# Performance work log

Hardware: AMD Instinct MI355X
Metric: run time of the kernel (lower is better)

Reference implementation:

```python
import jax, jax.numpy as jnp
import numpy as np

B, T, I = 8, 128, 196
TEXT_DIM, IMAGE_DIM, HIDDEN = 768, 1024, 512


def setup_inputs() -> dict:
    key = jax.random.key(0)
    ks = jax.random.split(key, 7)
    s = lambda d: 1.0 / np.sqrt(d)
    return {
        "text_features": jax.random.normal(ks[0], (B, T, TEXT_DIM), jnp.float32),
        "image_features": jax.random.normal(ks[1], (B, I, IMAGE_DIM), jnp.float32),
        "Wt": jax.random.normal(ks[2], (TEXT_DIM, HIDDEN), jnp.float32) * s(TEXT_DIM),
        "bt": jax.random.normal(ks[3], (HIDDEN,), jnp.float32) * s(TEXT_DIM),
        "Wi": jax.random.normal(ks[4], (IMAGE_DIM, HIDDEN), jnp.float32) * s(IMAGE_DIM),
        "bi": jax.random.normal(ks[5], (HIDDEN,), jnp.float32) * s(IMAGE_DIM),
        "wa": jax.random.normal(ks[6], (HIDDEN,), jnp.float32) * s(HIDDEN),
        "ba": jnp.zeros((1,), jnp.float32),
    }


def reference(text_features, image_features, Wt, bt, Wi, bi, wa, ba):
    # projections: [B,T,H] and [B,I,H]
    pt = jnp.einsum("btd,dh->bth", text_features, Wt) + bt
    pi = jnp.einsum("bid,dh->bih", image_features, Wi) + bi
    # additive Bahdanau scores: tanh of broadcast sum [B,T,I,H], reduced by wa
    h = jnp.tanh(pt[:, :, None, :] + pi[:, None, :, :])
    scores = jnp.einsum("btih,h->bti", h, wa) + ba[0]  # [B,T,I]
    text_attended = jnp.einsum("bti,bid->btd", jax.nn.softmax(scores, axis=-1), image_features)
    image_attended = jnp.einsum("bti,btd->bid", jax.nn.softmax(scores, axis=1), text_features)
    return text_attended, image_attended
```

## Files before the change

kernel.cpp:

```cpp
#include <hip/hip_runtime.h>
#include <math.h>

#define B 8
#define T 128
#define I_TOK 196
#define TEXT_DIM 768
#define IMAGE_DIM 1024
#define HIDDEN 512
#define EXP_SCALE 2.88539008177792681f

#if __has_builtin(__builtin_amdgcn_exp2f)
#define FAST_EXP2(x) __builtin_amdgcn_exp2f(x)
#else
#define FAST_EXP2(x) exp2f(x)
#endif
#if __has_builtin(__builtin_amdgcn_rcpf)
#define FAST_RCP(x) __builtin_amdgcn_rcpf(x)
#else
#define FAST_RCP(x) __fdividef(1.f, (x))
#endif
#if __has_builtin(__builtin_amdgcn_sched_barrier)
#define SCHED_FENCE() __builtin_amdgcn_sched_barrier(0)
#else
#define SCHED_FENCE()
#endif

typedef short bf16x8 __attribute__((ext_vector_type(8)));
typedef float f32x4 __attribute__((ext_vector_type(4)));

#define KT_T (TEXT_DIM / 32)
#define KT_I (IMAGE_DIM / 32)
#define MT_T (B * T / 16)
#define MT_I (B * I_TOK / 16)
#define NT   (HIDDEN / 16)

#define XT_ELEMS (MT_T * KT_T * 512)
#define XI_ELEMS (MT_I * KT_I * 512)
#define X_ELEMS  (XT_ELEMS + XI_ELEMS)
#define WT_T_ELEMS (NT * KT_T * 512)
#define W_ELEMS (WT_T_ELEMS + NT * KT_I * 512)

#define XTILES_T (MT_T * KT_T)
#define XTILES   (XTILES_T + MT_I * KT_I)
#define WTILES_T (NT * KT_T)
#define WTILES   (WTILES_T + NT * KT_I)
#define PREP_GRID ((XTILES + WTILES) / 4)

__device__ __forceinline__ unsigned short f2bf(float x) {
    unsigned int u = __float_as_uint(x);
    unsigned int r = u + 0x7FFFu + ((u >> 16) & 1u);
    return (unsigned short)(r >> 16);
}
__device__ __forceinline__ float bf2f(unsigned short h) {
    return __uint_as_float(((unsigned int)h) << 16);
}

__global__ __launch_bounds__(256) void prep_kernel(
        const float* __restrict__ text, const float* __restrict__ image,
        const float* __restrict__ Wt, const float* __restrict__ Wi,
        unsigned short* __restrict__ Xh, unsigned short* __restrict__ Xl,
        unsigned short* __restrict__ WTh, unsigned short* __restrict__ WTl)
{
    const int tid = threadIdx.x;
    const int lane = tid & 63, wv = tid >> 6;
    const int r16 = lane & 15, quad = lane >> 4;
    const int id = blockIdx.x * 4 + wv;

    float v[8];
    unsigned short* oh;
    unsigned short* ol;
    long dst;

    if (id < XTILES) {
        const float* X; int K, mt, kt;
        if (id < XTILES_T) { X = text; K = TEXT_DIM; mt = id / KT_T; kt = id % KT_T; }
        else { const int i2 = id - XTILES_T; X = image; K = IMAGE_DIM; mt = i2 / KT_I; kt = i2 % KT_I; }
        const float* src = X + (long)(mt * 16 + r16) * K + kt * 32 + quad * 8;
        const float4 a = *(const float4*)src;
        const float4 b = *(const float4*)(src + 4);
        v[0]=a.x; v[1]=a.y; v[2]=a.z; v[3]=a.w; v[4]=b.x; v[5]=b.y; v[6]=b.z; v[7]=b.w;
        oh = (id < XTILES_T) ? Xh : Xh + XT_ELEMS;
        ol = (id < XTILES_T) ? Xl : Xl + XT_ELEMS;
        const long tile = (id < XTILES_T) ? id : (long)(id - XTILES_T);
        dst = tile * 512 + lane * 8;
    } else {
        const int idw = id - XTILES;
        const float* W; int K, nt, kt;
        if (idw < WTILES_T) { W = Wt; K = TEXT_DIM; nt = idw / KT_T; kt = idw % KT_T; }
        else { const int i2 = idw - WTILES_T; W = Wi; K = IMAGE_DIM; nt = i2 / KT_I; kt = i2 % KT_I; }
        const float* src = W + (long)(kt * 32 + quad * 8) * HIDDEN + nt * 16 + r16;
        #pragma unroll
        for (int j = 0; j < 8; ++j) v[j] = src[(long)j * HIDDEN];
        oh = (idw < WTILES_T) ? WTh : WTh + WT_T_ELEMS;
        ol = (idw < WTILES_T) ? WTl : WTl + WT_T_ELEMS;
        const long tile = (idw < WTILES_T) ? idw : (long)(idw - WTILES_T);
        dst = tile * 512 + lane * 8;
    }

    uint4 hv, lv;
    unsigned int hh[8], ll[8];
    #pragma unroll
    for (int j = 0; j < 8; ++j) {
        hh[j] = f2bf(v[j]);
        ll[j] = f2bf(v[j] - bf2f((unsigned short)hh[j]));
    }
    hv.x = hh[0] | (hh[1] << 16); hv.y = hh[2] | (hh[3] << 16);
    hv.z = hh[4] | (hh[5] << 16); hv.w = hh[6] | (hh[7] << 16);
    lv.x = ll[0] | (ll[1] << 16); lv.y = ll[2] | (ll[3] << 16);
    lv.z = ll[4] | (ll[5] << 16); lv.w = ll[6] | (ll[7] << 16);
    *(uint4*)(oh + dst) = hv;
    *(uint4*)(ol + dst) = lv;
}

#define GT_BLOCKS (32 * 8)
#define GI_BLOCKS (49 * 8)
#define GEMM_GRID (GT_BLOCKS + GI_BLOCKS)
#define PSTRIDE 66

__global__ __launch_bounds__(256, 2) void mfma_proj_kernel(
        const unsigned short* __restrict__ Xh, const unsigned short* __restrict__ Xl,
        const unsigned short* __restrict__ WTh, const unsigned short* __restrict__ WTl,
        const float* __restrict__ bt, const float* __restrict__ bi,
        float* __restrict__ pt, float* __restrict__ pi)
{
    __shared__ float part[32 * PSTRIDE];

    const int tid = threadIdx.x;
    const int lane = tid & 63, wv = tid >> 6;
    const int r16 = lane & 15, quad = lane >> 4;
    const int nh = wv & 1;
    const int kh = wv >> 1;

    int bid = blockIdx.x;
    const unsigned short *xh, *xl, *wh, *wl; const float* bias; float* Y;
    int ktiles;
    if (bid < GT_BLOCKS) {
        xh = Xh; xl = Xl; wh = WTh; wl = WTl; bias = bt; Y = pt; ktiles = KT_T;
    } else {
        bid -= GT_BLOCKS;
        xh = Xh + XT_ELEMS; xl = Xl + XT_ELEMS;
        wh = WTh + WT_T_ELEMS; wl = WTl + WT_T_ELEMS;
        bias = bi; Y = pi; ktiles = KT_I;
    }
    const int m0 = (bid >> 3) * 32;
    const int n0 = (bid & 7) * 64 + nh * 32;
    const int nstep = ktiles >> 1;
    const int kt0 = kh * nstep;
    const int mt0 = (bid >> 3) * 2;
    const int nt0 = (bid & 7) * 4 + nh * 2;

    const unsigned short* pa0 = xh + ((long)mt0 * ktiles + kt0) * 512 + lane * 8;
    const unsigned short* pa1 = pa0 + (long)ktiles * 512;
    const unsigned short* qa0 = xl + ((long)mt0 * ktiles + kt0) * 512 + lane * 8;
    const unsigned short* qa1 = qa0 + (long)ktiles * 512;
    const unsigned short* pb0 = wh + ((long)nt0 * ktiles + kt0) * 512 + lane * 8;
    const unsigned short* pb1 = pb0 + (long)ktiles * 512;
    const unsigned short* qb0 = wl + ((long)nt0 * ktiles + kt0) * 512 + lane * 8;
    const unsigned short* qb1 = qb0 + (long)ktiles * 512;

    f32x4 a00 = {0,0,0,0}, a01 = {0,0,0,0}, a10 = {0,0,0,0}, a11 = {0,0,0,0};

    bf16x8 Ah0 = *(const bf16x8*)(pa0);
    bf16x8 Ah1 = *(const bf16x8*)(pa1);
    bf16x8 Al0 = *(const bf16x8*)(qa0);
    bf16x8 Al1 = *(const bf16x8*)(qa1);
    bf16x8 Bh0 = *(const bf16x8*)(pb0);
    bf16x8 Bh1 = *(const bf16x8*)(pb1);
    bf16x8 Bl0 = *(const bf16x8*)(qb0);
    bf16x8 Bl1 = *(const bf16x8*)(qb1);

    for (int s = 0; s < nstep; ++s) {
        const long kn = (s + 1 < nstep) ? (long)(s + 1) * 512 : 0;
        const bf16x8 nAh0 = *(const bf16x8*)(pa0 + kn);
        const bf16x8 nAh1 = *(const bf16x8*)(pa1 + kn);
        const bf16x8 nAl0 = *(const bf16x8*)(qa0 + kn);
        const bf16x8 nAl1 = *(const bf16x8*)(qa1 + kn);
        const bf16x8 nBh0 = *(const bf16x8*)(pb0 + kn);
        const bf16x8 nBh1 = *(const bf16x8*)(pb1 + kn);
        const bf16x8 nBl0 = *(const bf16x8*)(qb0 + kn);
        const bf16x8 nBl1 = *(const bf16x8*)(qb1 + kn);
        SCHED_FENCE();

        a00 = __builtin_amdgcn_mfma_f32_16x16x32_bf16(Ah0, Bh0, a00, 0, 0, 0);
        a01 = __builtin_amdgcn_mfma_f32_16x16x32_bf16(Ah0, Bh1, a01, 0, 0, 0);
        a10 = __builtin_amdgcn_mfma_f32_16x16x32_bf16(Ah1, Bh0, a10, 0, 0, 0);
        a11 = __builtin_amdgcn_mfma_f32_16x16x32_bf16(Ah1, Bh1, a11, 0, 0, 0);
        a00 = __builtin_amdgcn_mfma_f32_16x16x32_bf16(Ah0, Bl0, a00, 0, 0, 0);
        a01 = __builtin_amdgcn_mfma_f32_16x16x32_bf16(Ah0, Bl1, a01, 0, 0, 0);
        a10 = __builtin_amdgcn_mfma_f32_16x16x32_bf16(Ah1, Bl0, a10, 0, 0, 0);
        a11 = __builtin_amdgcn_mfma_f32_16x16x32_bf16(Ah1, Bl1, a11, 0, 0, 0);
        a00 = __builtin_amdgcn_mfma_f32_16x16x32_bf16(Al0, Bh0, a00, 0, 0, 0);
        a01 = __builtin_amdgcn_mfma_f32_16x16x32_bf16(Al0, Bh1, a01, 0, 0, 0);
        a10 = __builtin_amdgcn_mfma_f32_16x16x32_bf16(Al1, Bh0, a10, 0, 0, 0);
        a11 = __builtin_amdgcn_mfma_f32_16x16x32_bf16(Al1, Bh1, a11, 0, 0, 0);
        SCHED_FENCE();

        Ah0 = nAh0; Ah1 = nAh1; Al0 = nAl0; Al1 = nAl1;
        Bh0 = nBh0; Bh1 = nBh1; Bl0 = nBl0; Bl1 = nBl1;
    }

    const int lc = nh * 32 + r16;
    if (kh == 1) {
        #pragma unroll
        for (int r = 0; r < 4; ++r) {
            part[(quad * 4 + r) * PSTRIDE + lc]           = a00[r];
            part[(quad * 4 + r) * PSTRIDE + lc + 16]      = a01[r];
            part[(quad * 4 + 16 + r) * PSTRIDE + lc]      = a10[r];
            part[(quad * 4 + 16 + r) * PSTRIDE + lc + 16] = a11[r];
        }
    }
    __syncthreads();
    if (kh == 0) {
        const int row0 = m0 + quad * 4;
        const float bv0 = bias[n0 + r16];
        const float bv1 = bias[n0 + 16 + r16];
        #pragma unroll
        for (int r = 0; r < 4; ++r) {
            const float v00 = (a00[r] + part[(quad * 4 + r) * PSTRIDE + lc]           + bv0) * EXP_SCALE;
            const float v01 = (a01[r] + part[(quad * 4 + r) * PSTRIDE + lc + 16]      + bv1) * EXP_SCALE;
            const float v10 = (a10[r] + part[(quad * 4 + 16 + r) * PSTRIDE + lc]      + bv0) * EXP_SCALE;
            const float v11 = (a11[r] + part[(quad * 4 + 16 + r) * PSTRIDE + lc + 16] + bv1) * EXP_SCALE;
            Y[(long)(row0 + r)      * HIDDEN + n0 + r16]      = FAST_EXP2(v00);
            Y[(long)(row0 + r)      * HIDDEN + n0 + 16 + r16] = FAST_EXP2(v01);
            Y[(long)(row0 + 16 + r) * HIDDEN + n0 + r16]      = FAST_EXP2(v10);
            Y[(long)(row0 + 16 + r) * HIDDEN + n0 + 16 + r16] = FAST_EXP2(v11);
        }
    }
}

__global__ __launch_bounds__(256, 8) void scores_kernel(const float* __restrict__ pt,
        const float* __restrict__ pi, const float* __restrict__ wa,
        const float* __restrict__ ba, float* __restrict__ scores)
{
    const int blk = blockIdx.x;
    const int bt = blk >> 1;
    const int half = blk & 1;
    const int b = bt >> 7;
    const int tid = threadIdx.x;
    const int lane = tid & 63, wave = tid >> 6;

    const float* ptrow = pt + (long)bt * HIDDEN + lane * 8;
    const float4 pA = *(const float4*)ptrow;
    const float4 pB = *(const float4*)(ptrow + 4);
    float4 wA = *(const float4*)(wa + lane * 8);
    float4 wB = *(const float4*)(wa + lane * 8 + 4);

    float S = wA.x + wA.y + wA.z + wA.w + wB.x + wB.y + wB.z + wB.w;
    #pragma unroll
    for (int off = 32; off; off >>= 1) S += __shfl_down(S, off);
    const float base = S + ba[0];

    wA.x *= -2.f; wA.y *= -2.f; wA.z *= -2.f; wA.w *= -2.f;
    wB.x *= -2.f; wB.y *= -2.f; wB.z *= -2.f; wB.w *= -2.f;

    const float* pib = pi + (long)b * I_TOK * HIDDEN + lane * 8;
    const int i0 = half * 98 + wave;
    const int iend = half * 98 + 98;

    float4 ca = *(const float4*)(pib + (long)i0 * HIDDEN);
    float4 cb = *(const float4*)(pib + (long)i0 * HIDDEN + 4);

    for (int i = i0; i < iend; i += 4) {
        const int inx = (i + 4 < iend) ? (i + 4) : i;
        const float4 na = *(const float4*)(pib + (long)inx * HIDDEN);
        const float4 nb = *(const float4*)(pib + (long)inx * HIDDEN + 4);

        float acc = 0.f;
        acc = fmaf(wA.x, FAST_RCP(fmaf(pA.x, ca.x, 1.f)), acc);
        acc = fmaf(wA.y, FAST_RCP(fmaf(pA.y, ca.y, 1.f)), acc);
        acc = fmaf(wA.z, FAST_RCP(fmaf(pA.z, ca.z, 1.f)), acc);
        acc = fmaf(wA.w, FAST_RCP(fmaf(pA.w, ca.w, 1.f)), acc);
        acc = fmaf(wB.x, FAST_RCP(fmaf(pB.x, cb.x, 1.f)), acc);
        acc = fmaf(wB.y, FAST_RCP(fmaf(pB.y, cb.y, 1.f)), acc);
        acc = fmaf(wB.z, FAST_RCP(fmaf(pB.z, cb.z, 1.f)), acc);
        acc = fmaf(wB.w, FAST_RCP(fmaf(pB.w, cb.w, 1.f)), acc);

        #pragma unroll
        for (int off = 32; off; off >>= 1) acc += __shfl_down(acc, off);
        if (lane == 0) scores[(long)bt * I_TOK + i] = base + acc;
        ca = na; cb = nb;
    }
}

__global__ __launch_bounds__(256) void att_kernel(const float* __restrict__ scores,
        const float* __restrict__ image, const float* __restrict__ text,
        float* __restrict__ out_text, float* __restrict__ out_img)
{
    const int tid = threadIdx.x, lane = tid & 63, wave = tid >> 6;

    if (blockIdx.x < 512) {
        const int bid = blockIdx.x;
        const int csplit = bid & 1;
        const int grp = bid >> 1;
        const int b = grp >> 5;
        const int t0 = (grp & 31) * 4;

        __shared__ float ps[I_TOK][4];
        {
            const float* srow = scores + ((long)(b * T + t0 + wave)) * I_TOK;
            const float s0 = srow[lane];
            const float s1 = srow[lane + 64];
            const float s2 = srow[lane + 128];
            const float s3 = (lane < 4) ? srow[lane + 192] : -INFINITY;
            float m = fmaxf(fmaxf(s0, s1), fmaxf(s2, s3));
            #pragma unroll
            for (int off = 32; off; off >>= 1) m = fmaxf(m, __shfl_xor(m, off));
            const float e0 = __expf(s0 - m);
            const float e1 = __expf(s1 - m);
            const float e2 = __expf(s2 - m);
            const float e3 = (lane < 4) ? __expf(s3 - m) : 0.f;
            float sum = e0 + e1 + e2 + e3;
            #pragma unroll
            for (int off = 32; off; off >>= 1) sum += __shfl_xor(sum, off);
            const float inv = __fdividef(1.0f, sum);
            ps[lane][wave] = e0 * inv;
            ps[lane + 64][wave] = e1 * inv;
            ps[lane + 128][wave] = e2 * inv;
            if (lane < 4) ps[lane + 192][wave] = e3 * inv;
        }
        __syncthreads();

        const float* img = image + (long)b * I_TOK * IMAGE_DIM + csplit * 512 + tid * 2;
        float a00 = 0.f, a01 = 0.f, a10 = 0.f, a11 = 0.f;
        float a20 = 0.f, a21 = 0.f, a30 = 0.f, a31 = 0.f;

        float2 v0 = *(const float2*)(img + 0 * IMAGE_DIM);
        float2 v1 = *(const float2*)(img + 1 * IMAGE_DIM);
        float2 v2 = *(const float2*)(img + 2 * IMAGE_DIM);
        float2 v3 = *(const float2*)(img + 3 * IMAGE_DIM);
        float4 p0 = *(const float4*)&ps[0][0];
        float4 p1 = *(const float4*)&ps[1][0];
        float4 p2 = *(const float4*)&ps[2][0];
        float4 p3 = *(const float4*)&ps[3][0];

        for (int g = 0; g < 49; ++g) {
            const int ib = (g + 1 < 49) ? (g + 1) * 4 : g * 4;
            const float2 w0 = *(const float2*)(img + (long)(ib + 0) * IMAGE_DIM);
            const float2 w1 = *(const float2*)(img + (long)(ib + 1) * IMAGE_DIM);
            const float2 w2 = *(const float2*)(img + (long)(ib + 2) * IMAGE_DIM);
            const float2 w3 = *(const float2*)(img + (long)(ib + 3) * IMAGE_DIM);
            const float4 r0 = *(const float4*)&ps[ib + 0][0];
            const float4 r1 = *(const float4*)&ps[ib + 1][0];
            const float4 r2 = *(const float4*)&ps[ib + 2][0];
            const float4 r3 = *(const float4*)&ps[ib + 3][0];
            a00 = fmaf(p0.x, v0.x, a00); a01 = fmaf(p0.x, v0.y, a01);
            a10 = fmaf(p0.y, v0.x, a10); a11 = fmaf(p0.y, v0.y, a11);
            a20 = fmaf(p0.z, v0.x, a20); a21 = fmaf(p0.z, v0.y, a21);
            a30 = fmaf(p0.w, v0.x, a30); a31 = fmaf(p0.w, v0.y, a31);
            a00 = fmaf(p1.x, v1.x, a00); a01 = fmaf(p1.x, v1.y, a01);
            a10 = fmaf(p1.y, v1.x, a10); a11 = fmaf(p1.y, v1.y, a11);
            a20 = fmaf(p1.z, v1.x, a20); a21 = fmaf(p1.z, v1.y, a21);
            a30 = fmaf(p1.w, v1.x, a30); a31 = fmaf(p1.w, v1.y, a31);
            a00 = fmaf(p2.x, v2.x, a00); a01 = fmaf(p2.x, v2.y, a01);
            a10 = fmaf(p2.y, v2.x, a10); a11 = fmaf(p2.y, v2.y, a11);
            a20 = fmaf(p2.z, v2.x, a20); a21 = fmaf(p2.z, v2.y, a21);
            a30 = fmaf(p2.w, v2.x, a30); a31 = fmaf(p2.w, v2.y, a31);
            a00 = fmaf(p3.x, v3.x, a00); a01 = fmaf(p3.x, v3.y, a01);
            a10 = fmaf(p3.y, v3.x, a10); a11 = fmaf(p3.y, v3.y, a11);
            a20 = fmaf(p3.z, v3.x, a20); a21 = fmaf(p3.z, v3.y, a21);
            a30 = fmaf(p3.w, v3.x, a30); a31 = fmaf(p3.w, v3.y, a31);
            v0 = w0; v1 = w1; v2 = w2; v3 = w3;
            p0 = r0; p1 = r1; p2 = r2; p3 = r3;
        }
        float* o = out_text + ((long)(b * T + t0)) * IMAGE_DIM + csplit * 512 + tid * 2;
        float2 w;
        w.x = a00; w.y = a01; *(float2*)(o + 0 * IMAGE_DIM) = w;
        w.x = a10; w.y = a11; *(float2*)(o + 1 * IMAGE_DIM) = w;
        w.x = a20; w.y = a21; *(float2*)(o + 2 * IMAGE_DIM) = w;
        w.x = a30; w.y = a31; *(float2*)(o + 3 * IMAGE_DIM) = w;
    } else {
        const int bid = blockIdx.x - 512;
        const int b = bid / (I_TOK / 4);
        const int i0 = (bid % (I_TOK / 4)) * 4;

        __shared__ float qs[T][4];
        {
            const float* sc = scores + (long)b * T * I_TOK + (i0 + wave);
            const float s0 = sc[(long)lane * I_TOK];
            const float s1 = sc[(long)(lane + 64) * I_TOK];
            float m = fmaxf(s0, s1);
            #pragma unroll
            for (int off = 32; off; off >>= 1) m = fmaxf(m, __shfl_xor(m, off));
            const float e0 = __expf(s0 - m);
            const float e1 = __expf(s1 - m);
            float sum = e0 + e1;
            #pragma unroll
            for (int off = 32; off; off >>= 1) sum += __shfl_xor(sum, off);
            const float inv = __fdividef(1.0f, sum);
            qs[lane][wave] = e0 * inv;
            qs[lane + 64][wave] = e1 * inv;
        }
        __syncthreads();

        const float* txt2 = text + (long)b * T * TEXT_DIM + tid * 2;
        const float* txt1 = text + (long)b * T * TEXT_DIM + 512 + tid;
        float a00=0.f,a01=0.f,a02=0.f, a10=0.f,a11=0.f,a12=0.f;
        float a20=0.f,a21=0.f,a22=0.f, a30=0.f,a31=0.f,a32=0.f;

        float2 u0 = *(const float2*)(txt2 + 0 * TEXT_DIM);
        float2 u1 = *(const float2*)(txt2 + 1 * TEXT_DIM);
        float  z0 = txt1[0 * TEXT_DIM];
        float  z1 = txt1[1 * TEXT_DIM];
        float4 q0 = *(const float4*)&qs[0][0];
        float4 q1 = *(const float4*)&qs[1][0];

        for (int g = 0; g < 64; ++g) {
            const int tb = (g + 1 < 64) ? (g + 1) * 2 : g * 2;
            const float2 nu0 = *(const float2*)(txt2 + (long)(tb + 0) * TEXT_DIM);
            const float2 nu1 = *(const float2*)(txt2 + (long)(tb + 1) * TEXT_DIM);
            const float  nz0 = txt1[(long)(tb + 0) * TEXT_DIM];
            const float  nz1 = txt1[(long)(tb + 1) * TEXT_DIM];
            const float4 nq0 = *(const float4*)&qs[tb + 0][0];
            const float4 nq1 = *(const float4*)&qs[tb + 1][0];
            a00 = fmaf(q0.x, u0.x, a00); a01 = fmaf(q0.x, u0.y, a01); a02 = fmaf(q0.x, z0, a02);
            a10 = fmaf(q0.y, u0.x, a10); a11 = fmaf(q0.y, u0.y, a11); a12 = fmaf(q0.y, z0, a12);
            a20 = fmaf(q0.z, u0.x, a20); a21 = fmaf(q0.z, u0.y, a21); a22 = fmaf(q0.z, z0, a22);
            a30 = fmaf(q0.w, u0.x, a30); a31 = fmaf(q0.w, u0.y, a31); a32 = fmaf(q0.w, z0, a32);
            a00 = fmaf(q1.x, u1.x, a00); a01 = fmaf(q1.x, u1.y, a01); a02 = fmaf(q1.x, z1, a02);
            a10 = fmaf(q1.y, u1.x, a10); a11 = fmaf(q1.y, u1.y, a11); a12 = fmaf(q1.y, z1, a12);
            a20 = fmaf(q1.z, u1.x, a20); a21 = fmaf(q1.z, u1.y, a21); a22 = fmaf(q1.z, z1, a22);
            a30 = fmaf(q1.w, u1.x, a30); a31 = fmaf(q1.w, u1.y, a31); a32 = fmaf(q1.w, z1, a32);
            u0 = nu0; u1 = nu1; z0 = nz0; z1 = nz1; q0 = nq0; q1 = nq1;
        }
        float* o = out_img + ((long)b * I_TOK + i0) * TEXT_DIM;
        float2 w;
        w.x = a00; w.y = a01; *(float2*)(o + 0 * TEXT_DIM + tid * 2) = w; o[0 * TEXT_DIM + 512 + tid] = a02;
        w.x = a10; w.y = a11; *(float2*)(o + 1 * TEXT_DIM + tid * 2) = w; o[1 * TEXT_DIM + 512 + tid] = a12;
        w.x = a20; w.y = a21; *(float2*)(o + 2 * TEXT_DIM + tid * 2) = w; o[2 * TEXT_DIM + 512 + tid] = a22;
        w.x = a30; w.y = a31; *(float2*)(o + 3 * TEXT_DIM + tid * 2) = w; o[3 * TEXT_DIM + 512 + tid] = a32;
    }
}

extern "C" void kernel_launch(void* const* d_in, const int* in_sizes, int n_in,
                              void* d_out, int out_size, void* d_ws, size_t ws_size,
                              hipStream_t stream) {
    const float* text  = (const float*)d_in[0];
    const float* image = (const float*)d_in[1];
    const float* Wt    = (const float*)d_in[2];
    const float* bt    = (const float*)d_in[3];
    const float* Wi    = (const float*)d_in[4];
    const float* bi    = (const float*)d_in[5];
    const float* wa    = (const float*)d_in[6];
    const float* ba    = (const float*)d_in[7];

    float* pt = (float*)d_ws;
    float* pi = pt + (long)B * T * HIDDEN;
    float* sc = pi + (long)B * I_TOK * HIDDEN;
    unsigned short* Xh  = (unsigned short*)(sc + (long)B * T * I_TOK);
    unsigned short* Xl  = Xh + X_ELEMS;
    unsigned short* WTh = Xl + X_ELEMS;
    unsigned short* WTl = WTh + W_ELEMS;

    float* out_text = (float*)d_out;
    float* out_img  = out_text + (long)B * T * IMAGE_DIM;

    prep_kernel<<<PREP_GRID, 256, 0, stream>>>(text, image, Wt, Wi, Xh, Xl, WTh, WTl);
    mfma_proj_kernel<<<GEMM_GRID, 256, 0, stream>>>(Xh, Xl, WTh, WTl, bt, bi, pt, pi);
    scores_kernel<<<2 * B * T, 256, 0, stream>>>(pt, pi, wa, ba, sc);
    att_kernel<<<512 + B * (I_TOK / 4), 256, 0, stream>>>(sc, image, text, out_text, out_img);
}
```

Measured before the change: 145.5 us.

## Process two text rows per scores block and widen attention output tiles

The scores kernel now computes two text rows per block, so each loaded image-projection vector is reused twice, which halves the grid and pi traffic. The occupancy hint drops from 8 to 4 blocks per CU to leave room for the extra registers. The attention kernel now gives each block 8 text rows (was 4) and 7 image tokens (was 4), which cuts redundant re-reads of image and text features. The cost is more registers per thread and fewer blocks to keep the GPU busy.

```diff
diff --git a/kernel.cpp b/kernel.cpp
--- a/kernel.cpp
+++ b/kernel.cpp
@@ -228,20 +228,22 @@
     }
 }
 
-__global__ __launch_bounds__(256, 8) void scores_kernel(const float* __restrict__ pt,
+__global__ __launch_bounds__(256, 4) void scores_kernel(const float* __restrict__ pt,
         const float* __restrict__ pi, const float* __restrict__ wa,
         const float* __restrict__ ba, float* __restrict__ scores)
 {
     const int blk = blockIdx.x;
-    const int bt = blk >> 1;
     const int half = blk & 1;
-    const int b = bt >> 7;
+    const int bt0 = (blk >> 1) * 2;
+    const int b = bt0 >> 7;
     const int tid = threadIdx.x;
     const int lane = tid & 63, wave = tid >> 6;
 
-    const float* ptrow = pt + (long)bt * HIDDEN + lane * 8;
-    const float4 pA = *(const float4*)ptrow;
-    const float4 pB = *(const float4*)(ptrow + 4);
+    const float* ptrow = pt + (long)bt0 * HIDDEN + lane * 8;
+    const float4 pA0 = *(const float4*)ptrow;
+    const float4 pB0 = *(const float4*)(ptrow + 4);
+    const float4 pA1 = *(const float4*)(ptrow + HIDDEN);
+    const float4 pB1 = *(const float4*)(ptrow + HIDDEN + 4);
     float4 wA = *(const float4*)(wa + lane * 8);
     float4 wB = *(const float4*)(wa + lane * 8 + 4);
 
@@ -265,22 +267,42 @@
         const float4 na = *(const float4*)(pib + (long)inx * HIDDEN);
         const float4 nb = *(const float4*)(pib + (long)inx * HIDDEN + 4);
 
-        float acc = 0.f;
-        acc = fmaf(wA.x, FAST_RCP(fmaf(pA.x, ca.x, 1.f)), acc);
-        acc = fmaf(wA.y, FAST_RCP(fmaf(pA.y, ca.y, 1.f)), acc);
-        acc = fmaf(wA.z, FAST_RCP(fmaf(pA.z, ca.z, 1.f)), acc);
-        acc = fmaf(wA.w, FAST_RCP(fmaf(pA.w, ca.w, 1.f)), acc);
-        acc = fmaf(wB.x, FAST_RCP(fmaf(pB.x, cb.x, 1.f)), acc);
-        acc = fmaf(wB.y, FAST_RCP(fmaf(pB.y, cb.y, 1.f)), acc);
-        acc = fmaf(wB.z, FAST_RCP(fmaf(pB.z, cb.z, 1.f)), acc);
-        acc = fmaf(wB.w, FAST_RCP(fmaf(pB.w, cb.w, 1.f)), acc);
-
-        #pragma unroll
-        for (int off = 32; off; off >>= 1) acc += __shfl_down(acc, off);
-        if (lane == 0) scores[(long)bt * I_TOK + i] = base + acc;
+        float acc0 = 0.f;
+        acc0 = fmaf(wA.x, FAST_RCP(fmaf(pA0.x, ca.x, 1.f)), acc0);
+        acc0 = fmaf(wA.y, FAST_RCP(fmaf(pA0.y, ca.y, 1.f)), acc0);
+        acc0 = fmaf(wA.z, FAST_RCP(fmaf(pA0.z, ca.z, 1.f)), acc0);
+        acc0 = fmaf(wA.w, FAST_RCP(fmaf(pA0.w, ca.w, 1.f)), acc0);
+        acc0 = fmaf(wB.x, FAST_RCP(fmaf(pB0.x, cb.x, 1.f)), acc0);
+        acc0 = fmaf(wB.y, FAST_RCP(fmaf(pB0.y, cb.y, 1.f)), acc0);
+        acc0 = fmaf(wB.z, FAST_RCP(fmaf(pB0.z, cb.z, 1.f)), acc0);
+        acc0 = fmaf(wB.w, FAST_RCP(fmaf(pB0.w, cb.w, 1.f)), acc0);
+
+        float acc1 = 0.f;
+        acc1 = fmaf(wA.x, FAST_RCP(fmaf(pA1.x, ca.x, 1.f)), acc1);
+        acc1 = fmaf(wA.y, FAST_RCP(fmaf(pA1.y, ca.y, 1.f)), acc1);
+        acc1 = fmaf(wA.z, FAST_RCP(fmaf(pA1.z, ca.z, 1.f)), acc1);
+        acc1 = fmaf(wA.w, FAST_RCP(fmaf(pA1.w, ca.w, 1.f)), acc1);
+        acc1 = fmaf(wB.x, FAST_RCP(fmaf(pB1.x, cb.x, 1.f)), acc1);
+        acc1 = fmaf(wB.y, FAST_RCP(fmaf(pB1.y, cb.y, 1.f)), acc1);
+        acc1 = fmaf(wB.z, FAST_RCP(fmaf(pB1.z, cb.z, 1.f)), acc1);
+        acc1 = fmaf(wB.w, FAST_RCP(fmaf(pB1.w, cb.w, 1.f)), acc1);
+
+        #pragma unroll
+        for (int off = 32; off; off >>= 1) {
+            acc0 += __shfl_down(acc0, off);
+            acc1 += __shfl_down(acc1, off);
+        }
+        if (lane == 0) {
+            scores[(long)bt0 * I_TOK + i]       = base + acc0;
+            scores[(long)(bt0 + 1) * I_TOK + i] = base + acc1;
+        }
         ca = na; cb = nb;
     }
 }
+
+#define ATT_P1_BLOCKS 256
+#define ATT_P2_BLOCKS (B * 28)
+#define ATT_GRID (ATT_P1_BLOCKS + ATT_P2_BLOCKS)
 
 __global__ __launch_bounds__(256) void att_kernel(const float* __restrict__ scores,
         const float* __restrict__ image, const float* __restrict__ text,
@@ -288,16 +310,18 @@
 {
     const int tid = threadIdx.x, lane = tid & 63, wave = tid >> 6;
 
-    if (blockIdx.x < 512) {
+    if (blockIdx.x < ATT_P1_BLOCKS) {
         const int bid = blockIdx.x;
         const int csplit = bid & 1;
         const int grp = bid >> 1;
-        const int b = grp >> 5;
-        const int t0 = (grp & 31) * 4;
-
-        __shared__ float ps[I_TOK][4];
-        {
-            const float* srow = scores + ((long)(b * T + t0 + wave)) * I_TOK;
+        const int b = grp >> 4;
+        const int t0 = (grp & 15) * 8;
+
+        __shared__ float ps[I_TOK][8];
+        #pragma unroll
+        for (int rr = 0; rr < 2; ++rr) {
+            const int tsub = wave + rr * 4;
+            const float* srow = scores + ((long)(b * T + t0 + tsub)) * I_TOK;
             const float s0 = srow[lane];
             const float s1 = srow[lane + 64];
             const float s2 = srow[lane + 128];
@@ -313,25 +337,25 @@
             #pragma unroll
             for (int off = 32; off; off >>= 1) sum += __shfl_xor(sum, off);
             const float inv = __fdividef(1.0f, sum);
-            ps[lane][wave] = e0 * inv;
-            ps[lane + 64][wave] = e1 * inv;
-            ps[lane + 128][wave] = e2 * inv;
-            if (lane < 4) ps[lane + 192][wave] = e3 * inv;
+            ps[lane][tsub] = e0 * inv;
+            ps[lane + 64][tsub] = e1 * inv;
+            ps[lane + 128][tsub] = e2 * inv;
+            if (lane < 4) ps[lane + 192][tsub] = e3 * inv;
         }
         __syncthreads();
 
         const float* img = image + (long)b * I_TOK * IMAGE_DIM + csplit * 512 + tid * 2;
-        float a00 = 0.f, a01 = 0.f, a10 = 0.f, a11 = 0.f;
-        float a20 = 0.f, a21 = 0.f, a30 = 0.f, a31 = 0.f;
+        float2 a0 = {0,0}, a1 = {0,0}, a2 = {0,0}, a3 = {0,0};
+        float2 a4 = {0,0}, a5 = {0,0}, a6 = {0,0}, a7 = {0,0};
 
         float2 v0 = *(const float2*)(img + 0 * IMAGE_DIM);
         float2 v1 = *(const float2*)(img + 1 * IMAGE_DIM);
         float2 v2 = *(const float2*)(img + 2 * IMAGE_DIM);
         float2 v3 = *(const float2*)(img + 3 * IMAGE_DIM);
-        float4 p0 = *(const float4*)&ps[0][0];
-        float4 p1 = *(const float4*)&ps[1][0];
-        float4 p2 = *(const float4*)&ps[2][0];
-        float4 p3 = *(const float4*)&ps[3][0];
+        float4 pL0 = *(const float4*)&ps[0][0]; float4 pH0 = *(const float4*)&ps[0][4];
+        float4 pL1 = *(const float4*)&ps[1][0]; float4 pH1 = *(const float4*)&ps[1][4];
+        float4 pL2 = *(const float4*)&ps[2][0]; float4 pH2 = *(const float4*)&ps[2][4];
+        float4 pL3 = *(const float4*)&ps[3][0]; float4 pH3 = *(const float4*)&ps[3][4];
 
         for (int g = 0; g < 49; ++g) {
             const int ib = (g + 1 < 49) ? (g + 1) * 4 : g * 4;
@@ -339,43 +363,46 @@
             const float2 w1 = *(const float2*)(img + (long)(ib + 1) * IMAGE_DIM);
             const float2 w2 = *(const float2*)(img + (long)(ib + 2) * IMAGE_DIM);
             const float2 w3 = *(const float2*)(img + (long)(ib + 3) * IMAGE_DIM);
-            const float4 r0 = *(const float4*)&ps[ib + 0][0];
-            const float4 r1 = *(const float4*)&ps[ib + 1][0];
-            const float4 r2 = *(const float4*)&ps[ib + 2][0];
-            const float4 r3 = *(const float4*)&ps[ib + 3][0];
-            a00 = fmaf(p0.x, v0.x, a00); a01 = fmaf(p0.x, v0.y, a01);
-            a10 = fmaf(p0.y, v0.x, a10); a11 = fmaf(p0.y, v0.y, a11);
-            a20 = fmaf(p0.z, v0.x, a20); a21 = fmaf(p0.z, v0.y, a21);
-            a30 = fmaf(p0.w, v0.x, a30); a31 = fmaf(p0.w, v0.y, a31);
-            a00 = fmaf(p1.x, v1.x, a00); a01 = fmaf(p1.x, v1.y, a01);
-            a10 = fmaf(p1.y, v1.x, a10); a11 = fmaf(p1.y, v1.y, a11);
-            a20 = fmaf(p1.z, v1.x, a20); a21 = fmaf(p1.z, v1.y, a21);
-            a30 = fmaf(p1.w, v1.x, a30); a31 = fmaf(p1.w, v1.y, a31);
-            a00 = fmaf(p2.x, v2.x, a00); a01 = fmaf(p2.x, v2.y, a01);
-            a10 = fmaf(p2.y, v2.x, a10); a11 = fmaf(p2.y, v2.y, a11);
-            a20 = fmaf(p2.z, v2.x, a20); a21 = fmaf(p2.z, v2.y, a21);
-            a30 = fmaf(p2.w, v2.x, a30); a31 = fmaf(p2.w, v2.y, a31);
-            a00 = fmaf(p3.x, v3.x, a00); a01 = fmaf(p3.x, v3.y, a01);
-            a10 = fmaf(p3.y, v3.x, a10); a11 = fmaf(p3.y, v3.y, a11);
-            a20 = fmaf(p3.z, v3.x, a20); a21 = fmaf(p3.z, v3.y, a21);
-            a30 = fmaf(p3.w, v3.x, a30); a31 = fmaf(p3.w, v3.y, a31);
+            const float4 nL0 = *(const float4*)&ps[ib + 0][0]; const float4 nH0 = *(const float4*)&ps[ib + 0][4];
+            const float4 nL1 = *(const float4*)&ps[ib + 1][0]; const float4 nH1 = *(const float4*)&ps[ib + 1][4];
+            const float4 nL2 = *(const float4*)&ps[ib + 2][0]; const float4 nH2 = *(const float4*)&ps[ib + 2][4];
+            const float4 nL3 = *(const float4*)&ps[ib + 3][0]; const float4 nH3 = *(const float4*)&ps[ib + 3][4];
+
+#define ATT_ROW(vr, pl, ph)                                                   \
+            a0.x = fmaf(pl.x, vr.x, a0.x); a0.y = fmaf(pl.x, vr.y, a0.y);     \
+            a1.x = fmaf(pl.y, vr.x, a1.x); a1.y = fmaf(pl.y, vr.y, a1.y);     \
+            a2.x = fmaf(pl.z, vr.x, a2.x); a2.y = fmaf(pl.z, vr.y, a2.y);     \
+            a3.x = fmaf(pl.w, vr.x, a3.x); a3.y = fmaf(pl.w, vr.y, a3.y);     \
+            a4.x = fmaf(ph.x, vr.x, a4.x); a4.y = fmaf(ph.x, vr.y, a4.y);     \
+            a5.x = fmaf(ph.y, vr.x, a5.x); a5.y = fmaf(ph.y, vr.y, a5.y);     \
+            a6.x = fmaf(ph.z, vr.x, a6.x); a6.y = fmaf(ph.z, vr.y, a6.y);     \
+            a7.x = fmaf(ph.w, vr.x, a7.x); a7.y = fmaf(ph.w, vr.y, a7.y);
+            ATT_ROW(v0, pL0, pH0)
+            ATT_ROW(v1, pL1, pH1)
+            ATT_ROW(v2, pL2, pH2)
+            ATT_ROW(v3, pL3, pH3)
+#undef ATT_ROW
             v0 = w0; v1 = w1; v2 = w2; v3 = w3;
-            p0 = r0; p1 = r1; p2 = r2; p3 = r3;
+            pL0 = nL0; pH0 = nH0; pL1 = nL1; pH1 = nH1;
+            pL2 = nL2; pH2 = nH2; pL3 = nL3; pH3 = nH3;
         }
         float* o = out_text + ((long)(b * T + t0)) * IMAGE_DIM + csplit * 512 + tid * 2;
-        float2 w;
-        w.x = a00; w.y = a01; *(float2*)(o + 0 * IMAGE_DIM) = w;
-        w.x = a10; w.y = a11; *(float2*)(o + 1 * IMAGE_DIM) = w;
-        w.x = a20; w.y = a21; *(float2*)(o + 2 * IMAGE_DIM) = w;
-        w.x = a30; w.y = a31; *(float2*)(o + 3 * IMAGE_DIM) = w;
+        *(float2*)(o + 0 * IMAGE_DIM) = a0;
+        *(float2*)(o + 1 * IMAGE_DIM) = a1;
+        *(float2*)(o + 2 * IMAGE_DIM) = a2;
+        *(float2*)(o + 3 * IMAGE_DIM) = a3;
+        *(float2*)(o + 4 * IMAGE_DIM) = a4;
+        *(float2*)(o + 5 * IMAGE_DIM) = a5;
+        *(float2*)(o + 6 * IMAGE_DIM) = a6;
+        *(float2*)(o + 7 * IMAGE_DIM) = a7;
     } else {
-        const int bid = blockIdx.x - 512;
-        const int b = bid / (I_TOK / 4);
-        const int i0 = (bid % (I_TOK / 4)) * 4;
-
-        __shared__ float qs[T][4];
-        {
-            const float* sc = scores + (long)b * T * I_TOK + (i0 + wave);
+        const int bid = blockIdx.x - ATT_P1_BLOCKS;
+        const int b = bid / 28;
+        const int i0 = (bid % 28) * 7;
+
+        __shared__ float qs[T][8];
+        for (int cc = wave; cc < 7; cc += 4) {
+            const float* sc = scores + (long)b * T * I_TOK + (i0 + cc);
             const float s0 = sc[(long)lane * I_TOK];
             const float s1 = sc[(long)(lane + 64) * I_TOK];
             float m = fmaxf(s0, s1);
@@ -387,22 +414,23 @@
             #pragma unroll
             for (int off = 32; off; off >>= 1) sum += __shfl_xor(sum, off);
             const float inv = __fdividef(1.0f, sum);
-            qs[lane][wave] = e0 * inv;
-            qs[lane + 64][wave] = e1 * inv;
+            qs[lane][cc] = e0 * inv;
+            qs[lane + 64][cc] = e1 * inv;
         }
         __syncthreads();
 
         const float* txt2 = text + (long)b * T * TEXT_DIM + tid * 2;
         const float* txt1 = text + (long)b * T * TEXT_DIM + 512 + tid;
-        float a00=0.f,a01=0.f,a02=0.f, a10=0.f,a11=0.f,a12=0.f;
-        float a20=0.f,a21=0.f,a22=0.f, a30=0.f,a31=0.f,a32=0.f;
+        float ax[7], ay[7], az[7];
+        #pragma unroll
+        for (int r = 0; r < 7; ++r) { ax[r] = 0.f; ay[r] = 0.f; az[r] = 0.f; }
 
         float2 u0 = *(const float2*)(txt2 + 0 * TEXT_DIM);
         float2 u1 = *(const float2*)(txt2 + 1 * TEXT_DIM);
         float  z0 = txt1[0 * TEXT_DIM];
         float  z1 = txt1[1 * TEXT_DIM];
-        float4 q0 = *(const float4*)&qs[0][0];
-        float4 q1 = *(const float4*)&qs[1][0];
+        float4 qa0 = *(const float4*)&qs[0][0]; float4 qb0 = *(const float4*)&qs[0][4];
+        float4 qa1 = *(const float4*)&qs[1][0]; float4 qb1 = *(const float4*)&qs[1][4];
 
         for (int g = 0; g < 64; ++g) {
             const int tb = (g + 1 < 64) ? (g + 1) * 2 : g * 2;
@@ -410,24 +438,37 @@
             const float2 nu1 = *(const float2*)(txt2 + (long)(tb + 1) * TEXT_DIM);
             const float  nz0 = txt1[(long)(tb + 0) * TEXT_DIM];
             const float  nz1 = txt1[(long)(tb + 1) * TEXT_DIM];
-            const float4 nq0 = *(const float4*)&qs[tb + 0][0];
-            const float4 nq1 = *(const float4*)&qs[tb + 1][0];
-            a00 = fmaf(q0.x, u0.x, a00); a01 = fmaf(q0.x, u0.y, a01); a02 = fmaf(q0.x, z0, a02);
-            a10 = fmaf(q0.y, u0.x, a10); a11 = fmaf(q0.y, u0.y, a11); a12 = fmaf(q0.y, z0, a12);
-            a20 = fmaf(q0.z, u0.x, a20); a21 = fmaf(q0.z, u0.y, a21); a22 = fmaf(q0.z, z0, a22);
-            a30 = fmaf(q0.w, u0.x, a30); a31 = fmaf(q0.w, u0.y, a31); a32 = fmaf(q0.w, z0, a32);
-            a00 = fmaf(q1.x, u1.x, a00); a01 = fmaf(q1.x, u1.y, a01); a02 = fmaf(q1.x, z1, a02);
-            a10 = fmaf(q1.y, u1.x, a10); a11 = fmaf(q1.y, u1.y, a11); a12 = fmaf(q1.y, z1, a12);
-            a20 = fmaf(q1.z, u1.x, a20); a21 = fmaf(q1.z, u1.y, a21); a22 = fmaf(q1.z, z1, a22);
-            a30 = fmaf(q1.w, u1.x, a30); a31 = fmaf(q1.w, u1.y, a31); a32 = fmaf(q1.w, z1, a32);
-            u0 = nu0; u1 = nu1; z0 = nz0; z1 = nz1; q0 = nq0; q1 = nq1;
+            const float4 na0 = *(const float4*)&qs[tb + 0][0];
+            const float4 nb0 = *(const float4*)&qs[tb + 0][4];
+            const float4 na1 = *(const float4*)&qs[tb + 1][0];
+            const float4 nb1 = *(const float4*)&qs[tb + 1][4];
+
+            ax[0] = fmaf(qa0.x, u0.x, ax[0]); ay[0] = fmaf(qa0.x, u0.y, ay[0]); az[0] = fmaf(qa0.x, z0, az[0]);
+            ax[1] = fmaf(qa0.y, u0.x, ax[1]); ay[1] = fmaf(qa0.y, u0.y, ay[1]); az[1] = fmaf(qa0.y, z0, az[1]);
+            ax[2] = fmaf(qa0.z, u0.x, ax[2]); ay[2] = fmaf(qa0.z, u0.y, ay[2]); az[2] = fmaf(qa0.z, z0, az[2]);
+            ax[3] = fmaf(qa0.w, u0.x, ax[3]); ay[3] = fmaf(qa0.w, u0.y, ay[3]); az[3] = fmaf(qa0.w, z0, az[3]);
+            ax[4] = fmaf(qb0.x, u0.x, ax[4]); ay[4] = fmaf(qb0.x, u0.y, ay[4]); az[4] = fmaf(qb0.x, z0, az[4]);
+            ax[5] = fmaf(qb0.y, u0.x, ax[5]); ay[5] = fmaf(qb0.y, u0.y, ay[5]); az[5] = fmaf(qb0.y, z0, az[5]);
+            ax[6] = fmaf(qb0.z, u0.x, ax[6]); ay[6] = fmaf(qb0.z, u0.y, ay[6]); az[6] = fmaf(qb0.z, z0, az[6]);
+            ax[0] = fmaf(qa1.x, u1.x, ax[0]); ay[0] = fmaf(qa1.x, u1.y, ay[0]); az[0] = fmaf(qa1.x, z1, az[0]);
+            ax[1] = fmaf(qa1.y, u1.x, ax[1]); ay[1] = fmaf(qa1.y, u1.y, ay[1]); az[1] = fmaf(qa1.y, z1, az[1]);
+            ax[2] = fmaf(qa1.z, u1.x, ax[2]); ay[2] = fmaf(qa1.z, u1.y, ay[2]); az[2] = fmaf(qa1.z, z1, az[2]);
+            ax[3] = fmaf(qa1.w, u1.x, ax[3]); ay[3] = fmaf(qa1.w, u1.y, ay[3]); az[3] = fmaf(qa1.w, z1, az[3]);
+            ax[4] = fmaf(qb1.x, u1.x, ax[4]); ay[4] = fmaf(qb1.x, u1.y, ay[4]); az[4] = fmaf(qb1.x, z1, az[4]);
+            ax[5] = fmaf(qb1.y, u1.x, ax[5]); ay[5] = fmaf(qb1.y, u1.y, ay[5]); az[5] = fmaf(qb1.y, z1, az[5]);
+            ax[6] = fmaf(qb1.z, u1.x, ax[6]); ay[6] = fmaf(qb1.z, u1.y, ay[6]); az[6] = fmaf(qb1.z, z1, az[6]);
+
+            u0 = nu0; u1 = nu1; z0 = nz0; z1 = nz1;
+            qa0 = na0; qb0 = nb0; qa1 = na1; qb1 = nb1;
         }
         float* o = out_img + ((long)b * I_TOK + i0) * TEXT_DIM;
-        float2 w;
-        w.x = a00; w.y = a01; *(float2*)(o + 0 * TEXT_DIM + tid * 2) = w; o[0 * TEXT_DIM + 512 + tid] = a02;
-        w.x = a10; w.y = a11; *(float2*)(o + 1 * TEXT_DIM + tid * 2) = w; o[1 * TEXT_DIM + 512 + tid] = a12;
-        w.x = a20; w.y = a21; *(float2*)(o + 2 * TEXT_DIM + tid * 2) = w; o[2 * TEXT_DIM + 512 + tid] = a22;
-        w.x = a30; w.y = a31; *(float2*)(o + 3 * TEXT_DIM + tid * 2) = w; o[3 * TEXT_DIM + 512 + tid] = a32;
+        #pragma unroll
+        for (int r = 0; r < 7; ++r) {
+            float2 w;
+            w.x = ax[r]; w.y = ay[r];
+            *(float2*)(o + (long)r * TEXT_DIM + tid * 2) = w;
+            o[(long)r * TEXT_DIM + 512 + tid] = az[r];
+        }
     }
 }
 
@@ -456,6 +497,6 @@
 
     prep_kernel<<<PREP_GRID, 256, 0, stream>>>(text, image, Wt, Wi, Xh, Xl, WTh, WTl);
     mfma_proj_kernel<<<GEMM_GRID, 256, 0, stream>>>(Xh, Xl, WTh, WTl, bt, bi, pt, pi);
-    scores_kernel<<<2 * B * T, 256, 0, stream>>>(pt, pi, wa, ba, sc);
-    att_kernel<<<512 + B * (I_TOK / 4), 256, 0, stream>>>(sc, image, text, out_text, out_img);
-}
+    scores_kernel<<<B * T, 256, 0, stream>>>(pt, pi, wa, ba, sc);
+    att_kernel<<<ATT_GRID, 256, 0, stream>>>(sc, image, text, out_text, out_img);
+}
```

New measurement: 144.9 us. About the same (-0.5%).
